# Performance work log

Measured on AMD Instinct MI355X. Metric: run time of the kernel, lower is better.

## Reference

```python
import jax, jax.numpy as jnp
import numpy as np

NUM_HEAD = 16
D_Q = 512
D_KV = 512
ROPE_BASE = 10000.0


def _cos_sin(seq_len, dim):
    # Replicates calculate_cos_sin: theta = base**(-2*ids) / (dim//2)
    pos = jnp.arange(seq_len, dtype=jnp.float32)[:, None]          # (S,1)
    ids = jnp.arange(dim // 2, dtype=jnp.float32)                  # (D/2,)
    theta = (ROPE_BASE ** (-2.0 * ids)) / (dim // 2)
    r = pos * theta[None, :]                                       # (S, D/2)
    return jnp.cos(r), jnp.sin(r)


def _rope(x, cos, sin):
    b, s, d = x.shape
    xv = x.reshape(b, s, d // 2, 2)
    x0, x1 = xv[..., 0], xv[..., 1]
    out = jnp.stack([x0 * cos - x1 * sin, x1 * cos + x0 * sin], axis=-1)
    return out.reshape(b, s, d)


def setup_inputs() -> dict:
    key = jax.random.key(0)
    ks = jax.random.split(key, 10)
    d_model, d_q, d_kv = 1024, D_Q, D_KV
    b, s = 2, 2048
    w = lambda k, i, o: jax.random.normal(k, (i, o), dtype=jnp.float32) * 0.02
    return {
        "x": jax.random.normal(ks[0], (b, s, d_model), dtype=jnp.float32),
        "Wd_q_w": w(ks[1], d_model, d_q), "Wd_q_b": jnp.zeros((d_q,), jnp.float32),
        "Wu_q_w": w(ks[2], d_q, d_model), "Wu_q_b": jnp.zeros((d_model,), jnp.float32),
        "Wq_r_w": w(ks[3], d_q, d_model), "Wq_r_b": jnp.zeros((d_model,), jnp.float32),
        "Wk_r_w": w(ks[4], d_model, d_model), "Wk_r_b": jnp.zeros((d_model,), jnp.float32),
        "Wd_kv_w": w(ks[5], d_model, d_kv), "Wd_kv_b": jnp.zeros((d_kv,), jnp.float32),
        "Wu_k_w": w(ks[6], d_kv, d_model), "Wu_k_b": jnp.zeros((d_model,), jnp.float32),
        "Wu_v_w": w(ks[7], d_kv, d_model), "Wu_v_b": jnp.zeros((d_model,), jnp.float32),
        "Wo_w": w(ks[8], d_model, d_model), "Wo_b": jnp.zeros((d_model,), jnp.float32),
    }


def reference(x, Wd_q_w, Wd_q_b, Wu_q_w, Wu_q_b, Wq_r_w, Wq_r_b,
              Wk_r_w, Wk_r_b, Wd_kv_w, Wd_kv_b, Wu_k_w, Wu_k_b,
              Wu_v_w, Wu_v_b, Wo_w, Wo_b):
    b, s, d_model = x.shape
    h = NUM_HEAD
    hd = d_model // h
    scale = jnp.sqrt(jnp.float32(h + D_KV + D_Q))

    def heads(t):  # (b,s,d) -> (b,h,s,hd)
        return t.reshape(b, s, h, hd).transpose(0, 2, 1, 3)

    cos, sin = _cos_sin(s, d_model)

    ct_q = x @ Wd_q_w + Wd_q_b                                   # (b,s,d_q)
    qt_c = heads(ct_q @ Wu_q_w + Wu_q_b)
    qt_r = heads(_rope(ct_q @ Wq_r_w + Wq_r_b, cos, sin))
    query = qt_c + qt_r                                          # (b,h,s,hd)

    ct_kv = x @ Wd_kv_w + Wd_kv_b                                # (b,s,d_kv)
    kt_c = heads(ct_kv @ Wu_k_w + Wu_k_b)
    kt_r = heads(_rope(x @ Wk_r_w + Wk_r_b, cos, sin))
    key = kt_c + kt_r
    value = heads(ct_kv @ Wu_v_w + Wu_v_b)

    attn = jnp.einsum('bhqd,bhkd->bhqk', query, key) / scale
    attn = jax.nn.softmax(attn, axis=-1)
    out = jnp.einsum('bhqk,bhkd->bhqd', attn, value)
    out = out.transpose(0, 2, 1, 3).reshape(b, s, d_model)
    return out @ Wo_w + Wo_b
```

## Files before the change

### kernel.cpp

```cpp
#include <hip/hip_runtime.h>
#include <hip/hip_bf16.h>
#include <math.h>
#include <limits.h>

typedef __hip_bfloat16 bf16;
typedef __bf16 bf16x8 __attribute__((ext_vector_type(8)));
typedef float  f32x4  __attribute__((ext_vector_type(4)));

#define DEVI __device__ __forceinline__

static constexpr int Bb     = 2;
static constexpr int Ss     = 2048;
static constexpr int DMODEL = 1024;
static constexpr int NTOK   = Bb * Ss;

DEVI float bf2f(bf16 v) { return __bfloat162float(v); }
DEVI bf16  f2bf(float v) { return __float2bfloat16(v); }

DEVI unsigned int packbf(float lo, float hi) {
  union { bf16 b; unsigned short u; } a, c;
  a.b = f2bf(lo); c.b = f2bf(hi);
  return ((unsigned int)c.u << 16) | a.u;
}
DEVI float bfu2f(unsigned short u) {
  unsigned int x = (unsigned int)u << 16;
  float f; __builtin_memcpy(&f, &x, 4); return f;
}

DEVI void async_load16(const bf16* g, bf16* l) {
  __builtin_amdgcn_global_load_lds((const __attribute__((address_space(1))) void*)g,
                                   (__attribute__((address_space(3))) void*)l, 16, 0, 0);
}

struct TransDesc { const float* src; bf16* dst; int R; int C; int tstart; };
struct TransPack { TransDesc d[8]; };

__global__ __launch_bounds__(256) void trans_conv_kernel(
    TransPack p, const float* __restrict__ cx, bf16* __restrict__ cxo, int tstartConv) {
  __shared__ bf16 tl[64][65];
  const int t = blockIdx.x;
  if (t >= tstartConv) {
    const int idx = (t - tstartConv) * 256 + threadIdx.x;
    const float4 v = ((const float4*)cx)[idx];
    uint2 o; o.x = packbf(v.x, v.y); o.y = packbf(v.z, v.w);
    *(uint2*)&cxo[(size_t)idx * 4] = o;
    return;
  }
  int i = 0;
#pragma unroll
  for (int j = 1; j < 8; ++j) if (t >= p.d[j].tstart) i = j;
  const float* __restrict__ in = p.d[i].src;
  bf16* __restrict__ out = p.d[i].dst;
  const int R = p.d[i].R, C = p.d[i].C;
  const int rel = t - p.d[i].tstart;
  const int tilesC = C >> 6;
  const int r0 = (rel / tilesC) * 64, c0 = (rel % tilesC) * 64;
  const int tc = threadIdx.x & 63, tr = threadIdx.x >> 6;
#pragma unroll
  for (int q = 0; q < 16; ++q) {
    int r = tr + q * 4;
    tl[r][tc] = f2bf(in[(size_t)(r0 + r) * C + c0 + tc]);
  }
  __syncthreads();
#pragma unroll
  for (int q = 0; q < 16; ++q) {
    int r = tr + q * 4;
    out[(size_t)(c0 + r) * R + r0 + tc] = tl[tc][r];
  }
}

struct GemmDesc {
  const bf16* A; const bf16* WT; const float* b1; const float* b2; const bf16* ropeAdd; bf16* C;
  int lda, ldb, ldc, K, bsplit, nTX, blkStart, biasRow;
};
struct GemmBatch { GemmDesc d[4]; };

__global__ __launch_bounds__(256) void gemm_batch_kernel(GemmBatch gb) {
  const int t = blockIdx.x;
  int di = 0;
#pragma unroll
  for (int j = 1; j < 4; ++j) if (t >= gb.d[j].blkStart) di = j;
  const GemmDesc D = gb.d[di];
  const int rel = t - D.blkStart;
  const int tileN = (rel % D.nTX) * 128;
  const int tileM = (rel / D.nTX) * 128;

  __shared__ bf16 ldsA[128 * 32];
  __shared__ bf16 ldsB[128 * 32];
  const int tid = threadIdx.x;
  const int lane = tid & 63;
  const int w = tid >> 6;
  const int wr = w >> 1, wc = w & 1;
  const int l15 = lane & 15, lg = lane >> 4;
  const int lrow = lane >> 2;
  const int lcol = (lane & 3) * 8;

  f32x4 acc[4][4] = {};

  for (int k0 = 0; k0 < D.K; k0 += 32) {
    async_load16(D.A  + (size_t)(tileM + w * 32 +      lrow) * D.lda + k0 + lcol, &ldsA[(w * 32) * 32]);
    async_load16(D.A  + (size_t)(tileM + w * 32 + 16 + lrow) * D.lda + k0 + lcol, &ldsA[(w * 32 + 16) * 32]);
    async_load16(D.WT + (size_t)(tileN + w * 32 +      lrow) * D.ldb + k0 + lcol, &ldsB[(w * 32) * 32]);
    async_load16(D.WT + (size_t)(tileN + w * 32 + 16 + lrow) * D.ldb + k0 + lcol, &ldsB[(w * 32 + 16) * 32]);
    __syncthreads();

    bf16x8 af[4], bfr[4];
#pragma unroll
    for (int i = 0; i < 4; ++i) {
      af[i]  = *(const bf16x8*)&ldsA[(wr * 64 + i * 16 + l15) * 32 + lg * 8];
      bfr[i] = *(const bf16x8*)&ldsB[(wc * 64 + i * 16 + l15) * 32 + lg * 8];
    }
#pragma unroll
    for (int i = 0; i < 4; ++i)
#pragma unroll
      for (int j = 0; j < 4; ++j)
        acc[i][j] = __builtin_amdgcn_mfma_f32_16x16x32_bf16(af[i], bfr[j], acc[i][j], 0, 0, 0);
    __syncthreads();
  }

  const int mbase = tileM + wr * 64;
  const int nbase = tileN + wc * 64;
#pragma unroll
  for (int j = 0; j < 4; ++j) {
    int col = nbase + j * 16 + l15;
    float bvc = D.biasRow ? 0.0f : (col < D.bsplit ? D.b1[col] : D.b2[col - D.bsplit]);
    if (D.ropeAdd) {
      const int pcol = col >> 1;
      const bool odd = (col & 1) != 0;
      const float th = exp2f(-26.5754247f * (float)pcol) * (1.0f / 512.0f);
#pragma unroll
      for (int i = 0; i < 4; ++i)
#pragma unroll
        for (int r = 0; r < 4; ++r) {
          int row = mbase + i * 16 + lg * 4 + r;
          int s = row & (Ss - 1);
          unsigned int pr = *(const unsigned int*)((const char*)D.ropeAdd +
                              (size_t)row * D.ldc * 2 + (size_t)(col & ~1) * 2);
          float ke = bfu2f((unsigned short)(pr & 0xffff));
          float ko = bfu2f((unsigned short)(pr >> 16));
          float c = 1.0f, sn = (float)s * th;
          if (pcol == 0) { float rr = (float)s * (1.0f / 512.0f); c = cosf(rr); sn = sinf(rr); }
          float add = odd ? (ko * c + ke * sn) : (ke * c - ko * sn);
          D.C[(size_t)row * D.ldc + col] = f2bf(acc[i][j][r] + bvc + add);
        }
    } else {
#pragma unroll
      for (int i = 0; i < 4; ++i)
#pragma unroll
        for (int r = 0; r < 4; ++r) {
          int row = mbase + i * 16 + lg * 4 + r;
          float bv = D.biasRow ? D.b1[row] : bvc;
          D.C[(size_t)row * D.ldc + col] = f2bf(acc[i][j][r] + bv);
        }
    }
  }
}

__global__ __launch_bounds__(256) void gemm_kernel_f32(
    const bf16* __restrict__ A, int lda,
    const bf16* __restrict__ WT, int ldb,
    const float* __restrict__ b1,
    float* __restrict__ Cout, int ldc, int K) {
  __shared__ bf16 ldsA[128 * 32];
  __shared__ bf16 ldsB[64 * 32];
  const int tid = threadIdx.x;
  const int lane = tid & 63;
  const int w = tid >> 6;
  const int tileM = blockIdx.y * 128;
  const int tileN = blockIdx.x * 64;
  const int l15 = lane & 15, lg = lane >> 4;
  const int lrow = lane >> 2;
  const int lcol = (lane & 3) * 8;

  f32x4 acc[2][4] = {};

  for (int k0 = 0; k0 < K; k0 += 32) {
    async_load16(A  + (size_t)(tileM + w * 32 +      lrow) * lda + k0 + lcol, &ldsA[(w * 32) * 32]);
    async_load16(A  + (size_t)(tileM + w * 32 + 16 + lrow) * lda + k0 + lcol, &ldsA[(w * 32 + 16) * 32]);
    async_load16(WT + (size_t)(tileN + w * 16 + lrow) * ldb + k0 + lcol, &ldsB[(w * 16) * 32]);
    __syncthreads();

    bf16x8 af[2], bfr[4];
#pragma unroll
    for (int i = 0; i < 2; ++i)
      af[i]  = *(const bf16x8*)&ldsA[(w * 32 + i * 16 + l15) * 32 + lg * 8];
#pragma unroll
    for (int j = 0; j < 4; ++j)
      bfr[j] = *(const bf16x8*)&ldsB[(j * 16 + l15) * 32 + lg * 8];
#pragma unroll
    for (int i = 0; i < 2; ++i)
#pragma unroll
      for (int j = 0; j < 4; ++j)
        acc[i][j] = __builtin_amdgcn_mfma_f32_16x16x32_bf16(af[i], bfr[j], acc[i][j], 0, 0, 0);
    __syncthreads();
  }

#pragma unroll
  for (int j = 0; j < 4; ++j) {
    int col = tileN + j * 16 + l15;
    float bvc = b1[col];
#pragma unroll
    for (int i = 0; i < 2; ++i)
#pragma unroll
      for (int r = 0; r < 4; ++r) {
        int row = tileM + w * 32 + i * 16 + lg * 4 + r;
        Cout[(size_t)row * ldc + col] = acc[i][j][r] + bvc;
      }
  }
}

__global__ __launch_bounds__(256) void attn_kernel(
    const bf16* __restrict__ Qcm, const bf16* __restrict__ Qrm,
    const bf16* __restrict__ Kn, const bf16* __restrict__ VT,
    bf16* __restrict__ AO) {
  const int bh = blockIdx.x, qt = blockIdx.y;
  const int b = bh >> 4, h = bh & 15;
  const int tid = threadIdx.x, lane = tid & 63, w = tid >> 6;
  const int q0 = qt * 128 + w * 32;
  const int l15 = lane & 15, lg = lane >> 4;
  const float SC2 = 0.044736075f;
  const float THR = 11.5415603f;

  __shared__ bf16 ldsK[2][64 * 64];
  __shared__ bf16 ldsV[2][64 * 64];
  __shared__ bf16 ldsP[4][32 * 64];

  const bf16* Kg = Kn + (size_t)(b * Ss) * DMODEL + h * 64;
  const bf16* Vg = VT + (size_t)(h * 64) * NTOK + b * Ss;

  const int r0 = tid >> 3;
  const int srcb = ((tid & 7) * 16) ^ ((r0 & 7) << 4);
  const char* kS0 = (const char*)(Kg + (size_t)r0 * DMODEL) + srcb;
  const char* kS1 = (const char*)(Kg + (size_t)(32 + r0) * DMODEL) + srcb;
  const char* vS0 = (const char*)(Vg + (size_t)r0 * NTOK) + srcb;
  const char* vS1 = (const char*)(Vg + (size_t)(32 + r0) * NTOK) + srcb;
  const ptrdiff_t kAdv = (ptrdiff_t)64 * DMODEL * 2;
  const ptrdiff_t vAdv = 128;

  bf16* kd0_b0 = &ldsK[0][w * 512]; bf16* kd1_b0 = &ldsK[0][2048 + w * 512];
  bf16* kd0_b1 = &ldsK[1][w * 512]; bf16* kd1_b1 = &ldsK[1][2048 + w * 512];
  bf16* vd0_b0 = &ldsV[0][w * 512]; bf16* vd1_b0 = &ldsV[0][2048 + w * 512];
  bf16* vd0_b1 = &ldsV[1][w * 512]; bf16* vd1_b1 = &ldsV[1][2048 + w * 512];

  auto stageTo = [&](bf16* kd0, bf16* kd1, bf16* vd0, bf16* vd1) {
    async_load16((const bf16*)kS0, kd0);
    async_load16((const bf16*)kS1, kd1);
    async_load16((const bf16*)vS0, vd0);
    async_load16((const bf16*)vS1, vd1);
    kS0 += kAdv; kS1 += kAdv; vS0 += vAdv; vS1 += vAdv;
  };

  stageTo(kd0_b0, kd1_b0, vd0_b0, vd1_b0);

  const int kswz = (l15 & 7) << 4;
  const int xA = (lg * 16) ^ kswz;
  const int xB = (64 + lg * 16) ^ kswz;
  const char* krA0 = (const char*)&ldsK[0][0] + l15 * 128 + xA;
  const char* krB0 = (const char*)&ldsK[0][0] + l15 * 128 + xB;
  const char* krA1 = (const char*)&ldsK[1][0] + l15 * 128 + xA;
  const char* krB1 = (const char*)&ldsK[1][0] + l15 * 128 + xB;
  const char* vrA0 = (const char*)&ldsV[0][0] + l15 * 128 + xA;
  const char* vrB0 = (const char*)&ldsV[0][0] + l15 * 128 + xB;
  const char* vrA1 = (const char*)&ldsV[1][0] + l15 * 128 + xA;
  const char* vrB1 = (const char*)&ldsV[1][0] + l15 * 128 + xB;

  char* Pw = (char*)&ldsP[w][0];
  char* pwr[4];
#pragma unroll
  for (int j = 0; j < 4; ++j) {
    const int chunk = (j * 2 + (lg >> 1)) ^ (l15 & 7);
    pwr[j] = Pw + l15 * 128 + chunk * 16 + (lg & 1) * 8;
  }
  const char* paA = Pw + l15 * 128 + xA;
  const char* paB = Pw + l15 * 128 + xB;

  const int p0 = h * 32 + lg * 4;
  float th[2][4];
#pragma unroll
  for (int kg = 0; kg < 2; ++kg)
#pragma unroll
    for (int pp = 0; pp < 4; ++pp)
      th[kg][pp] = exp2f(-26.5754247f * (float)(p0 + kg * 16 + pp)) * (1.0f / 512.0f);

  bf16x8 bq[2][2];
#pragma unroll
  for (int i = 0; i < 2; ++i) {
    const int s = q0 + i * 16 + l15;
    const size_t rowoff = (size_t)(b * Ss + s) * DMODEL + h * 64;
#pragma unroll
    for (int kg = 0; kg < 2; ++kg) {
      union { bf16x8 v; unsigned short u[8]; } gc, gr;
      union { bf16x8 v; unsigned int w2[4]; } qo;
      gc.v = *(const bf16x8*)&Qcm[rowoff + kg * 32 + lg * 8];
      gr.v = *(const bf16x8*)&Qrm[rowoff + kg * 32 + lg * 8];
#pragma unroll
      for (int pp = 0; pp < 4; ++pp) {
        float c = 1.0f, sn = (float)s * th[kg][pp];
        if (p0 + kg * 16 + pp == 0) { float rr = (float)s * (1.0f / 512.0f); c = cosf(rr); sn = sinf(rr); }
        float g0 = bfu2f(gr.u[2 * pp]), g1 = bfu2f(gr.u[2 * pp + 1]);
        qo.w2[pp] = packbf(bfu2f(gc.u[2 * pp])     + g0 * c - g1 * sn,
                           bfu2f(gc.u[2 * pp + 1]) + g1 * c + g0 * sn);
      }
      bq[i][kg] = qo.v;
    }
  }

  float m[2] = { 0.0f, 0.0f }, l[2] = { 0.0f, 0.0f };
  f32x4 accO[2][4] = {};

  auto body = [&](const char* krA, const char* krB, const char* vrA, const char* vrB) {
    f32x4 sa[4][2] = {};
    __builtin_amdgcn_s_setprio(1);
#pragma unroll
    for (int j = 0; j < 4; ++j) {
      bf16x8 ak0 = *(const bf16x8*)(krA + j * 2048);
      bf16x8 ak1 = *(const bf16x8*)(krB + j * 2048);
#pragma unroll
      for (int i = 0; i < 2; ++i) {
        sa[j][i] = __builtin_amdgcn_mfma_f32_16x16x32_bf16(ak0, bq[i][0], sa[j][i], 0, 0, 0);
        sa[j][i] = __builtin_amdgcn_mfma_f32_16x16x32_bf16(ak1, bq[i][1], sa[j][i], 0, 0, 0);
      }
    }
    __builtin_amdgcn_s_setprio(0);
#pragma unroll
    for (int i = 0; i < 2; ++i) {
      float pmaxr = -3.0e38f;
#pragma unroll
      for (int j = 0; j < 4; ++j)
#pragma unroll
        for (int r = 0; r < 4; ++r) pmaxr = fmaxf(pmaxr, sa[j][i][r]);
      if (__any(fmaf(pmaxr, SC2, -m[i]) > THR)) {
        float px = fmaxf(pmaxr, __shfl_xor(pmaxr, 16, 64));
        px = fmaxf(px, __shfl_xor(px, 32, 64));
        float mnew = fmaxf(m[i], px * SC2);
        float corr = __builtin_amdgcn_exp2f(m[i] - mnew);
        m[i] = mnew; l[i] *= corr;
        float cr[4];
#pragma unroll
        for (int r = 0; r < 4; ++r) cr[r] = __shfl(corr, lg * 4 + r, 64);
#pragma unroll
        for (int dj = 0; dj < 4; ++dj)
#pragma unroll
          for (int r = 0; r < 4; ++r) accO[i][dj][r] *= cr[r];
      }
      float p[4][4];
      float ts0 = 0.f, ts1 = 0.f;
#pragma unroll
      for (int j = 0; j < 4; ++j) {
#pragma unroll
        for (int r = 0; r < 4; ++r)
          p[j][r] = __builtin_amdgcn_exp2f(fmaf(sa[j][i][r], SC2, -m[i]));
        ts0 += p[j][0] + p[j][2];
        ts1 += p[j][1] + p[j][3];
      }
      float ts = ts0 + ts1;
      ts += __shfl_xor(ts, 16, 64);
      ts += __shfl_xor(ts, 32, 64);
      l[i] += ts;
#pragma unroll
      for (int j = 0; j < 4; ++j) {
        uint2 pw;
        pw.x = packbf(p[j][0], p[j][1]);
        pw.y = packbf(p[j][2], p[j][3]);
        *(uint2*)(pwr[j] + i * 2048) = pw;
      }
    }
    bf16x8 pa[2][2];
#pragma unroll
    for (int i = 0; i < 2; ++i) {
      pa[i][0] = *(const bf16x8*)(paA + i * 2048);
      pa[i][1] = *(const bf16x8*)(paB + i * 2048);
    }
    __builtin_amdgcn_s_setprio(1);
#pragma unroll
    for (int dj = 0; dj < 4; ++dj) {
      bf16x8 bv0 = *(const bf16x8*)(vrA + dj * 2048);
      bf16x8 bv1 = *(const bf16x8*)(vrB + dj * 2048);
#pragma unroll
      for (int i = 0; i < 2; ++i) {
        accO[i][dj] = __builtin_amdgcn_mfma_f32_16x16x32_bf16(pa[i][0], bv0, accO[i][dj], 0, 0, 0);
        accO[i][dj] = __builtin_amdgcn_mfma_f32_16x16x32_bf16(pa[i][1], bv1, accO[i][dj], 0, 0, 0);
      }
    }
    __builtin_amdgcn_s_setprio(0);
  };

  for (int tt = 0; tt < 16; ++tt) {
    __syncthreads();
    stageTo(kd0_b1, kd1_b1, vd0_b1, vd1_b1);
    body(krA0, krB0, vrA0, vrB0);
    __syncthreads();
    if (tt < 15) stageTo(kd0_b0, kd1_b0, vd0_b0, vd1_b0);
    body(krA1, krB1, vrA1, vrB1);
  }

#pragma unroll
  for (int i = 0; i < 2; ++i) {
    float linv[4];
#pragma unroll
    for (int r = 0; r < 4; ++r) linv[r] = 1.0f / __shfl(l[i], lg * 4 + r, 64);
#pragma unroll
    for (int dj = 0; dj < 4; ++dj)
#pragma unroll
      for (int r = 0; r < 4; ++r)
        AO[(size_t)(b * Ss + q0 + i * 16 + lg * 4 + r) * DMODEL + h * 64 + dj * 16 + l15] =
            f2bf(accO[i][dj][r] * linv[r]);
  }
}

extern "C" void kernel_launch(void* const* d_in, const int* in_sizes, int n_in,
                              void* d_out, int out_size, void* d_ws, size_t ws_size,
                              hipStream_t stream) {
  const float* x      = (const float*)d_in[0];
  const float* Wdq    = (const float*)d_in[1];  const float* Wdq_b  = (const float*)d_in[2];
  const float* Wuq    = (const float*)d_in[3];  const float* Wuq_b  = (const float*)d_in[4];
  const float* Wqr    = (const float*)d_in[5];  const float* Wqr_b  = (const float*)d_in[6];
  const float* Wkr    = (const float*)d_in[7];  const float* Wkr_b  = (const float*)d_in[8];
  const float* Wdkv   = (const float*)d_in[9];  const float* Wdkv_b = (const float*)d_in[10];
  const float* Wuk    = (const float*)d_in[11]; const float* Wuk_b  = (const float*)d_in[12];
  const float* Wuv    = (const float*)d_in[13]; const float* Wuv_b  = (const float*)d_in[14];
  const float* Wo     = (const float*)d_in[15]; const float* Wo_b   = (const float*)d_in[16];

  char* ws = (char*)d_ws;
  size_t off = 0;
  bf16* WdqT   = (bf16*)(ws + off); off += (size_t)512  * 1024 * 2;
  bf16* WdkvT  = (bf16*)(ws + off); off += (size_t)512  * 1024 * 2;
  bf16* WuqT   = (bf16*)(ws + off); off += (size_t)1024 * 512  * 2;
  bf16* WqrT   = (bf16*)(ws + off); off += (size_t)1024 * 512  * 2;
  bf16* WukT   = (bf16*)(ws + off); off += (size_t)1024 * 512  * 2;
  bf16* WuvT   = (bf16*)(ws + off); off += (size_t)1024 * 512  * 2;
  bf16* WkrT   = (bf16*)(ws + off); off += (size_t)1024 * 1024 * 2;
  bf16* WoT    = (bf16*)(ws + off); off += (size_t)1024 * 1024 * 2;
  bf16* x_bf   = (bf16*)(ws + off); off += (size_t)NTOK * 1024 * 2;
  bf16* ct     = (bf16*)(ws + off); off += (size_t)NTOK * 1024 * 2;
  bf16* Ga     = (bf16*)(ws + off); off += (size_t)NTOK * 1024 * 2;
  bf16* VTr    = (bf16*)(ws + off); off += (size_t)NTOK * 1024 * 2;
  bf16* Qn     = (bf16*)d_out;
  bf16* Kn     = (bf16*)d_out + (size_t)NTOK * DMODEL;
  bf16* AO     = Ga;
  (void)ws_size; (void)in_sizes; (void)n_in; (void)out_size;

  TransPack tp = {{
    { Wdq,  WdqT,  1024, 512,  0    },
    { Wdkv, WdkvT, 1024, 512,  128  },
    { Wuq,  WuqT,  512,  1024, 256  },
    { Wqr,  WqrT,  512,  1024, 384  },
    { Wuk,  WukT,  512,  1024, 512  },
    { Wuv,  WuvT,  512,  1024, 640  },
    { Wkr,  WkrT,  1024, 1024, 768  },
    { Wo,   WoT,   1024, 1024, 1024 },
  }};
  trans_conv_kernel<<<1280 + 4096, 256, 0, stream>>>(tp, x, x_bf, 1280);

  GemmBatch ba = {{
    { x_bf, WdqT, Wdq_b, Wdkv_b, 0, ct, 1024, 1024, 1024, 1024, 512,     8, 0,       0 },
    { x_bf, WkrT, Wkr_b, Wkr_b,  0, Kn, 1024, 1024, 1024, 1024, INT_MAX, 8, 256,     0 },
    { 0, 0, 0, 0, 0, 0, 0, 0, 0, 0, 0, 1, INT_MAX, 0 },
    { 0, 0, 0, 0, 0, 0, 0, 0, 0, 0, 0, 1, INT_MAX, 0 },
  }};
  gemm_batch_kernel<<<512, 256, 0, stream>>>(ba);

  GemmBatch bb = {{
    { ct,       WuqT,     Wuq_b, Wuq_b, 0,  Ga,  1024, 512,  1024, 512, INT_MAX, 8,  0,   0 },
    { ct,       WqrT,     Wqr_b, Wqr_b, 0,  Qn,  1024, 512,  1024, 512, INT_MAX, 8,  256, 0 },
    { ct + 512, WukT,     Wuk_b, Wuk_b, Kn, Kn,  1024, 512,  1024, 512, INT_MAX, 8,  512, 0 },
    { WuvT,     ct + 512, Wuv_b, Wuv_b, 0,  VTr, 512,  1024, NTOK, 512, INT_MAX, 32, 768, 1 },
  }};
  gemm_batch_kernel<<<1024, 256, 0, stream>>>(bb);

  attn_kernel<<<dim3(32, 16), 256, 0, stream>>>(Ga, Qn, Kn, VTr, AO);

  gemm_kernel_f32<<<dim3(16, 32), 256, 0, stream>>>(
      AO, 1024, WoT, 1024, Wo_b, (float*)d_out, 1024, 1024);
}
```

Before: 177.8 us.

## Fold Q rope projection into Wu_q by summing weights, fix up pair zero

With base 10000 and this theta formula, every rope pair except the first has cos≈1 and sin≈0, so rope is nearly identity for pairs p≥1. The change sums Wu_q and Wq_r (and their biases) into one weight, removing a whole 512x1024 GEMM and the rope work inside attention. A small fixup kernel recomputes the pair-0 rotation exactly. The K-rope epilogue drops the per-element sin terms for the same reason, and the attention softmax row-sum shuffles move out of the inner loop to the end. It depends on theta underflowing for the test's constants, and the per-column terms it drops are tiny but not exactly zero.

Result: faster. 168.0 us (-5.5%).

```diff
diff --git a/kernel.cpp b/kernel.cpp
--- a/kernel.cpp
+++ b/kernel.cpp
@@ -32,13 +32,20 @@
                                    (__attribute__((address_space(3))) void*)l, 16, 0, 0);
 }
 
-struct TransDesc { const float* src; bf16* dst; int R; int C; int tstart; };
+struct TransDesc { const float* src; const float* src2; bf16* dst; int R; int C; int tstart; };
 struct TransPack { TransDesc d[8]; };
 
 __global__ __launch_bounds__(256) void trans_conv_kernel(
-    TransPack p, const float* __restrict__ cx, bf16* __restrict__ cxo, int tstartConv) {
+    TransPack p, const float* __restrict__ cx, bf16* __restrict__ cxo, int tstartConv,
+    const float* __restrict__ ba1, const float* __restrict__ ba2,
+    float* __restrict__ bsum, int tstartB) {
   __shared__ bf16 tl[64][65];
   const int t = blockIdx.x;
+  if (t >= tstartB) {
+    const int j = (t - tstartB) * 256 + threadIdx.x;
+    bsum[j] = ba1[j] + ba2[j];
+    return;
+  }
   if (t >= tstartConv) {
     const int idx = (t - tstartConv) * 256 + threadIdx.x;
     const float4 v = ((const float4*)cx)[idx];
@@ -49,7 +56,8 @@
   int i = 0;
 #pragma unroll
   for (int j = 1; j < 8; ++j) if (t >= p.d[j].tstart) i = j;
-  const float* __restrict__ in = p.d[i].src;
+  const float* __restrict__ in  = p.d[i].src;
+  const float* __restrict__ in2 = p.d[i].src2;
   bf16* __restrict__ out = p.d[i].dst;
   const int R = p.d[i].R, C = p.d[i].C;
   const int rel = t - p.d[i].tstart;
@@ -59,7 +67,9 @@
 #pragma unroll
   for (int q = 0; q < 16; ++q) {
     int r = tr + q * 4;
-    tl[r][tc] = f2bf(in[(size_t)(r0 + r) * C + c0 + tc]);
+    float v = in[(size_t)(r0 + r) * C + c0 + tc];
+    if (in2) v += in2[(size_t)(r0 + r) * C + c0 + tc];
+    tl[r][tc] = f2bf(v);
   }
   __syncthreads();
 #pragma unroll
@@ -70,7 +80,7 @@
 }
 
 struct GemmDesc {
-  const bf16* A; const bf16* WT; const float* b1; const float* b2; const bf16* ropeAdd; bf16* C;
+  const bf16* A; const bf16* WT; const float* b1; const float* b2; const bf16* addm; bf16* C;
   int lda, ldb, ldc, K, bsplit, nTX, blkStart, biasRow;
 };
 struct GemmBatch { GemmDesc d[4]; };
@@ -124,23 +134,26 @@
   for (int j = 0; j < 4; ++j) {
     int col = nbase + j * 16 + l15;
     float bvc = D.biasRow ? 0.0f : (col < D.bsplit ? D.b1[col] : D.b2[col - D.bsplit]);
-    if (D.ropeAdd) {
+    if (D.addm) {
       const int pcol = col >> 1;
       const bool odd = (col & 1) != 0;
-      const float th = exp2f(-26.5754247f * (float)pcol) * (1.0f / 512.0f);
 #pragma unroll
       for (int i = 0; i < 4; ++i)
 #pragma unroll
         for (int r = 0; r < 4; ++r) {
           int row = mbase + i * 16 + lg * 4 + r;
-          int s = row & (Ss - 1);
-          unsigned int pr = *(const unsigned int*)((const char*)D.ropeAdd +
+          unsigned int pr = *(const unsigned int*)((const char*)D.addm +
                               (size_t)row * D.ldc * 2 + (size_t)(col & ~1) * 2);
           float ke = bfu2f((unsigned short)(pr & 0xffff));
           float ko = bfu2f((unsigned short)(pr >> 16));
-          float c = 1.0f, sn = (float)s * th;
-          if (pcol == 0) { float rr = (float)s * (1.0f / 512.0f); c = cosf(rr); sn = sinf(rr); }
-          float add = odd ? (ko * c + ke * sn) : (ke * c - ko * sn);
+          float add;
+          if (pcol == 0) {
+            float rr = (float)(row & (Ss - 1)) * (1.0f / 512.0f);
+            float c = cosf(rr), sn = sinf(rr);
+            add = odd ? (ko * c + ke * sn) : (ke * c - ko * sn);
+          } else {
+            add = odd ? ko : ke;
+          }
           D.C[(size_t)row * D.ldc + col] = f2bf(acc[i][j][r] + bvc + add);
         }
     } else {
@@ -209,10 +222,38 @@
   }
 }
 
+__global__ __launch_bounds__(256) void fixup_q_kernel(
+    const bf16* __restrict__ ct, const float* __restrict__ Wqr,
+    const float* __restrict__ Wqr_b, bf16* __restrict__ Q) {
+  const int row = blockIdx.x * 4 + (threadIdx.x >> 6);
+  const int lane = threadIdx.x & 63;
+  const bf16* cr = ct + (size_t)row * 1024 + lane * 8;
+  const float* wq = Wqr + (size_t)(lane * 8) * 1024;
+  float q0 = 0.f, q1 = 0.f;
+#pragma unroll
+  for (int e = 0; e < 8; ++e) {
+    float xv = bf2f(cr[e]);
+    q0 = fmaf(xv, wq[e * 1024 + 0], q0);
+    q1 = fmaf(xv, wq[e * 1024 + 1], q1);
+  }
+#pragma unroll
+  for (int d = 32; d >= 1; d >>= 1) {
+    q0 += __shfl_xor(q0, d, 64);
+    q1 += __shfl_xor(q1, d, 64);
+  }
+  if (lane == 0) {
+    const float Qr0 = q0 + Wqr_b[0], Qr1 = q1 + Wqr_b[1];
+    const float rr = (float)(row & (Ss - 1)) * (1.0f / 512.0f);
+    const float cm1 = cosf(rr) - 1.0f, sn = sinf(rr);
+    const size_t base = (size_t)row * DMODEL;
+    Q[base]     = f2bf(bf2f(Q[base])     + Qr0 * cm1 - Qr1 * sn);
+    Q[base + 1] = f2bf(bf2f(Q[base + 1]) + Qr1 * cm1 + Qr0 * sn);
+  }
+}
+
 __global__ __launch_bounds__(256) void attn_kernel(
-    const bf16* __restrict__ Qcm, const bf16* __restrict__ Qrm,
-    const bf16* __restrict__ Kn, const bf16* __restrict__ VT,
-    bf16* __restrict__ AO) {
+    const bf16* __restrict__ Qm, const bf16* __restrict__ Kn,
+    const bf16* __restrict__ VT, bf16* __restrict__ AO) {
   const int bh = blockIdx.x, qt = blockIdx.y;
   const int b = bh >> 4, h = bh & 15;
   const int tid = threadIdx.x, lane = tid & 63, w = tid >> 6;
@@ -274,35 +315,12 @@
   const char* paA = Pw + l15 * 128 + xA;
   const char* paB = Pw + l15 * 128 + xB;
 
-  const int p0 = h * 32 + lg * 4;
-  float th[2][4];
-#pragma unroll
-  for (int kg = 0; kg < 2; ++kg)
-#pragma unroll
-    for (int pp = 0; pp < 4; ++pp)
-      th[kg][pp] = exp2f(-26.5754247f * (float)(p0 + kg * 16 + pp)) * (1.0f / 512.0f);
-
   bf16x8 bq[2][2];
 #pragma unroll
   for (int i = 0; i < 2; ++i) {
-    const int s = q0 + i * 16 + l15;
-    const size_t rowoff = (size_t)(b * Ss + s) * DMODEL + h * 64;
-#pragma unroll
-    for (int kg = 0; kg < 2; ++kg) {
-      union { bf16x8 v; unsigned short u[8]; } gc, gr;
-      union { bf16x8 v; unsigned int w2[4]; } qo;
-      gc.v = *(const bf16x8*)&Qcm[rowoff + kg * 32 + lg * 8];
-      gr.v = *(const bf16x8*)&Qrm[rowoff + kg * 32 + lg * 8];
-#pragma unroll
-      for (int pp = 0; pp < 4; ++pp) {
-        float c = 1.0f, sn = (float)s * th[kg][pp];
-        if (p0 + kg * 16 + pp == 0) { float rr = (float)s * (1.0f / 512.0f); c = cosf(rr); sn = sinf(rr); }
-        float g0 = bfu2f(gr.u[2 * pp]), g1 = bfu2f(gr.u[2 * pp + 1]);
-        qo.w2[pp] = packbf(bfu2f(gc.u[2 * pp])     + g0 * c - g1 * sn,
-                           bfu2f(gc.u[2 * pp + 1]) + g1 * c + g0 * sn);
-      }
-      bq[i][kg] = qo.v;
-    }
+    const size_t rowoff = (size_t)(b * Ss + q0 + i * 16 + l15) * DMODEL + h * 64;
+    bq[i][0] = *(const bf16x8*)&Qm[rowoff + lg * 8];
+    bq[i][1] = *(const bf16x8*)&Qm[rowoff + 32 + lg * 8];
   }
 
   float m[2] = { 0.0f, 0.0f }, l[2] = { 0.0f, 0.0f };
@@ -344,18 +362,14 @@
           for (int r = 0; r < 4; ++r) accO[i][dj][r] *= cr[r];
       }
       float p[4][4];
-      float ts0 = 0.f, ts1 = 0.f;
-#pragma unroll
-      for (int j = 0; j < 4; ++j) {
-#pragma unroll
-        for (int r = 0; r < 4; ++r)
+      float ts = 0.f;
+#pragma unroll
+      for (int j = 0; j < 4; ++j)
+#pragma unroll
+        for (int r = 0; r < 4; ++r) {
           p[j][r] = __builtin_amdgcn_exp2f(fmaf(sa[j][i][r], SC2, -m[i]));
-        ts0 += p[j][0] + p[j][2];
-        ts1 += p[j][1] + p[j][3];
-      }
-      float ts = ts0 + ts1;
-      ts += __shfl_xor(ts, 16, 64);
-      ts += __shfl_xor(ts, 32, 64);
+          ts += p[j][r];
+        }
       l[i] += ts;
 #pragma unroll
       for (int j = 0; j < 4; ++j) {
@@ -396,9 +410,12 @@
 
 #pragma unroll
   for (int i = 0; i < 2; ++i) {
+    float lt = l[i];
+    lt += __shfl_xor(lt, 16, 64);
+    lt += __shfl_xor(lt, 32, 64);
     float linv[4];
 #pragma unroll
-    for (int r = 0; r < 4; ++r) linv[r] = 1.0f / __shfl(l[i], lg * 4 + r, 64);
+    for (int r = 0; r < 4; ++r) linv[r] = 1.0f / __shfl(lt, lg * 4 + r, 64);
 #pragma unroll
     for (int dj = 0; dj < 4; ++dj)
 #pragma unroll
@@ -425,8 +442,7 @@
   size_t off = 0;
   bf16* WdqT   = (bf16*)(ws + off); off += (size_t)512  * 1024 * 2;
   bf16* WdkvT  = (bf16*)(ws + off); off += (size_t)512  * 1024 * 2;
-  bf16* WuqT   = (bf16*)(ws + off); off += (size_t)1024 * 512  * 2;
-  bf16* WqrT   = (bf16*)(ws + off); off += (size_t)1024 * 512  * 2;
+  bf16* WuqqrT = (bf16*)(ws + off); off += (size_t)1024 * 512  * 2;
   bf16* WukT   = (bf16*)(ws + off); off += (size_t)1024 * 512  * 2;
   bf16* WuvT   = (bf16*)(ws + off); off += (size_t)1024 * 512  * 2;
   bf16* WkrT   = (bf16*)(ws + off); off += (size_t)1024 * 1024 * 2;
@@ -435,22 +451,23 @@
   bf16* ct     = (bf16*)(ws + off); off += (size_t)NTOK * 1024 * 2;
   bf16* Ga     = (bf16*)(ws + off); off += (size_t)NTOK * 1024 * 2;
   bf16* VTr    = (bf16*)(ws + off); off += (size_t)NTOK * 1024 * 2;
-  bf16* Qn     = (bf16*)d_out;
+  float* qsum_b= (float*)(ws + off); off += 1024 * 4;
   bf16* Kn     = (bf16*)d_out + (size_t)NTOK * DMODEL;
   bf16* AO     = Ga;
   (void)ws_size; (void)in_sizes; (void)n_in; (void)out_size;
 
   TransPack tp = {{
-    { Wdq,  WdqT,  1024, 512,  0    },
-    { Wdkv, WdkvT, 1024, 512,  128  },
-    { Wuq,  WuqT,  512,  1024, 256  },
-    { Wqr,  WqrT,  512,  1024, 384  },
-    { Wuk,  WukT,  512,  1024, 512  },
-    { Wuv,  WuvT,  512,  1024, 640  },
-    { Wkr,  WkrT,  1024, 1024, 768  },
-    { Wo,   WoT,   1024, 1024, 1024 },
+    { Wdq,  0,   WdqT,   1024, 512,  0    },
+    { Wdkv, 0,   WdkvT,  1024, 512,  128  },
+    { Wuq,  Wqr, WuqqrT, 512,  1024, 256  },
+    { Wuk,  0,   WukT,   512,  1024, 384  },
+    { Wuv,  0,   WuvT,   512,  1024, 512  },
+    { Wkr,  0,   WkrT,   1024, 1024, 640  },
+    { Wo,   0,   WoT,    1024, 1024, 896  },
+    { 0, 0, 0, 0, 0, 1 << 30 },
   }};
-  trans_conv_kernel<<<1280 + 4096, 256, 0, stream>>>(tp, x, x_bf, 1280);
+  trans_conv_kernel<<<1152 + 4096 + 4, 256, 0, stream>>>(
+      tp, x, x_bf, 1152, Wuq_b, Wqr_b, qsum_b, 1152 + 4096);
 
   GemmBatch ba = {{
     { x_bf, WdqT, Wdq_b, Wdkv_b, 0, ct, 1024, 1024, 1024, 1024, 512,     8, 0,       0 },
@@ -461,14 +478,16 @@
   gemm_batch_kernel<<<512, 256, 0, stream>>>(ba);
 
   GemmBatch bb = {{
-    { ct,       WuqT,     Wuq_b, Wuq_b, 0,  Ga,  1024, 512,  1024, 512, INT_MAX, 8,  0,   0 },
-    { ct,       WqrT,     Wqr_b, Wqr_b, 0,  Qn,  1024, 512,  1024, 512, INT_MAX, 8,  256, 0 },
-    { ct + 512, WukT,     Wuk_b, Wuk_b, Kn, Kn,  1024, 512,  1024, 512, INT_MAX, 8,  512, 0 },
-    { WuvT,     ct + 512, Wuv_b, Wuv_b, 0,  VTr, 512,  1024, NTOK, 512, INT_MAX, 32, 768, 1 },
+    { ct,       WuqqrT,   qsum_b, qsum_b, 0,  Ga,  1024, 512,  1024, 512, INT_MAX, 8,  0,   0 },
+    { ct + 512, WukT,     Wuk_b,  Wuk_b,  Kn, Kn,  1024, 512,  1024, 512, INT_MAX, 8,  256, 0 },
+    { WuvT,     ct + 512, Wuv_b,  Wuv_b,  0,  VTr, 512,  1024, NTOK, 512, INT_MAX, 32, 512, 1 },
+    { 0, 0, 0, 0, 0, 0, 0, 0, 0, 0, 0, 1, 1 << 30, 0 },
   }};
-  gemm_batch_kernel<<<1024, 256, 0, stream>>>(bb);
-
-  attn_kernel<<<dim3(32, 16), 256, 0, stream>>>(Ga, Qn, Kn, VTr, AO);
+  gemm_batch_kernel<<<768, 256, 0, stream>>>(bb);
+
+  fixup_q_kernel<<<NTOK / 4, 256, 0, stream>>>(ct, Wqr, Wqr_b, Ga);
+
+  attn_kernel<<<dim3(32, 16), 256, 0, stream>>>(Ga, Kn, VTr, AO);
 
   gemm_kernel_f32<<<dim3(16, 32), 256, 0, stream>>>(
       AO, 1024, WoT, 1024, Wo_b, (float*)d_out, 1024, 1024);
```
